# Performance work log

Hardware: AMD Instinct MI355X
Metric: run time of the kernel (lower is better)

The kernel has to match this reference:

```python
import jax, jax.numpy as jnp
import numpy as np
import math

NO, NR, E = 100000, 1000, 1000000
DO, DR, DE, H, OM = 64, 32, 4, 64, 32


def setup_inputs() -> dict:
    key = jax.random.key(0)
    ks = jax.random.split(key, 20)
    s = lambda k, sh: jax.random.normal(k, sh, dtype=jnp.float32) * 0.05
    inp = {
        'x_order': jax.random.normal(ks[0], (NO, DO), dtype=jnp.float32),
        'x_rider': jax.random.normal(ks[1], (NR, DR), dtype=jnp.float32),
        'edge_attr': jax.random.normal(ks[2], (E, DE), dtype=jnp.float32),
        'order_idx': jax.random.randint(ks[3], (E,), 0, NO),
        'rider_idx': jax.random.randint(ks[4], (E,), 0, NR),
        'omega_encoded': jax.random.normal(ks[5], (OM,), dtype=jnp.float32),
        # TransformerConv params (heads=1)
        'Wk': s(ks[6], (DO, H)), 'bk': jnp.zeros((H,), jnp.float32),
        'Wq': s(ks[7], (DR, H)), 'bq': jnp.zeros((H,), jnp.float32),
        'Wv': s(ks[8], (DO, H)), 'bv': jnp.zeros((H,), jnp.float32),
        'We': s(ks[9], (DE, H)),  # lin_edge, bias=False in PyG
        'Wskip': s(ks[10], (DR, H)), 'bskip': jnp.zeros((H,), jnp.float32),
        # order_proj
        'Wp': s(ks[11], (DO, H)), 'bp': jnp.zeros((H,), jnp.float32),
        # residual MLP: Linear(2H+OM,128) -> ReLU -> Linear(128,1)
        'W1': s(ks[12], (2 * H + OM, 128)), 'b1': jnp.zeros((128,), jnp.float32),
        'W2': s(ks[13], (128, 1)), 'b2': jnp.zeros((1,), jnp.float32),
    }
    return inp


def _segment_softmax(alpha, seg, num_segments):
    m = jax.ops.segment_max(alpha, seg, num_segments=num_segments)
    m = jnp.where(jnp.isfinite(m), m, 0.0)
    ex = jnp.exp(alpha - m[seg])
    denom = jax.ops.segment_sum(ex, seg, num_segments=num_segments)
    return ex / (denom[seg] + 1e-16)


def reference(x_order, x_rider, edge_attr, order_idx, rider_idx, omega_encoded,
              Wk, bk, Wq, bq, Wv, bv, We, Wskip, bskip, Wp, bp, W1, b1, W2, b2):
    scale = 1.0 / math.sqrt(H)
    # TransformerConv((order, rider) -> rider), heads=1, edge_dim
    q = x_rider @ Wq + bq            # [NR, H]
    k = x_order @ Wk + bk            # [NO, H]
    v = x_order @ Wv + bv            # [NO, H]
    e = edge_attr @ We               # [E, H]
    k_j = k[order_idx] + e           # [E, H]
    v_j = v[order_idx] + e           # [E, H]
    alpha = jnp.sum(q[rider_idx] * k_j, axis=-1) * scale  # [E]
    alpha = _segment_softmax(alpha, rider_idx, NR)
    agg = jax.ops.segment_sum(alpha[:, None] * v_j, rider_idx, num_segments=NR)  # [NR, H]
    rider_emb = agg + x_rider @ Wskip + bskip  # root/skip connection

    # edge scoring
    order_proj = x_order @ Wp + bp   # [NO, H]
    oe = order_proj[order_idx]       # [E, H]
    re = rider_emb[rider_idx]        # [E, H]
    dot = jnp.sum(oe * re, axis=-1) * scale  # [E]
    omega_expand = jnp.broadcast_to(omega_encoded[None, :], (oe.shape[0], OM))
    resid_in = jnp.concatenate([oe, re, omega_expand], axis=-1)  # [E, 2H+OM]
    hmid = jax.nn.relu(resid_in @ W1 + b1)
    resid = (hmid @ W2 + b2)[:, 0]
    return jnp.clip(dot + resid, -10.0, 10.0)
```

## Files before the change

### kernel.cpp

```cpp
#include <hip/hip_runtime.h>
#include <hip/hip_bf16.h>
#include <math.h>

#define NO_N 100000
#define NR_N 1000
#define E_N  1000000
#define SB     250
#define SCHUNK 4000
#define KVP_TILES 1563

typedef short bf16x8 __attribute__((ext_vector_type(8)));
typedef float floatx4 __attribute__((ext_vector_type(4)));

__device__ __forceinline__ unsigned short bfu(float x) {
    union { __hip_bfloat16 h; unsigned short u; } c;
    c.h = __float2bfloat16(x);
    return c.u;
}
__device__ __forceinline__ float bflo(unsigned int u) {
    return __uint_as_float(u << 16);
}
__device__ __forceinline__ float bfhi(unsigned int u) {
    return __uint_as_float(u & 0xffff0000u);
}

__global__ __launch_bounds__(256) void k_prep_rider(
    const float* __restrict__ xr,
    const float* __restrict__ Wq, const float* __restrict__ bq,
    const float* __restrict__ Wskip, const float* __restrict__ bskip,
    const float* __restrict__ We,
    float* __restrict__ q, float* __restrict__ skip, float* __restrict__ t)
{
    __shared__ float sx[4][32];
    __shared__ float sq[4][64];
    int tid = threadIdx.x;
    int rbase = blockIdx.x * 4;
    if (tid < 128) {
        int rl = tid >> 5, d = tid & 31;
        int r = rbase + rl;
        sx[rl][d] = (r < NR_N) ? xr[r * 32 + d] : 0.f;
    }
    __syncthreads();
    int rl = tid >> 6, h = tid & 63;
    int r = rbase + rl;
    float aq = bq[h], as = bskip[h];
    #pragma unroll 4
    for (int d = 0; d < 32; ++d) {
        float xv = sx[rl][d];
        aq += xv * Wq[d * 64 + h];
        as += xv * Wskip[d * 64 + h];
    }
    sq[rl][h] = aq;
    if (r < NR_N) { q[r * 64 + h] = aq; skip[r * 64 + h] = as; }
    __syncthreads();
    if (tid < 16) {
        int rl2 = tid >> 2, d = tid & 3;
        int r2 = rbase + rl2;
        float acc = 0.f;
        for (int hh = 0; hh < 64; ++hh) acc += We[d * 64 + hh] * sq[rl2][hh];
        if (r2 < NR_N) t[r2 * 4 + d] = acc;
    }
}

__global__ __launch_bounds__(128) void k_prep_b1eff(
    const float* __restrict__ W1, const float* __restrict__ b1,
    const float* __restrict__ omega, float* __restrict__ b1eff)
{
    int c = threadIdx.x;
    float acc = b1[c];
    #pragma unroll 4
    for (int j = 0; j < 32; ++j) acc += omega[j] * W1[(128 + j) * 128 + c];
    b1eff[c] = acc;
}

__global__ __launch_bounds__(256) void k_kvp(
    const float* __restrict__ x,
    const float* __restrict__ Wk, const float* __restrict__ bk,
    const float* __restrict__ Wv, const float* __restrict__ bv,
    const float* __restrict__ Wp, const float* __restrict__ bp,
    unsigned short* __restrict__ kb, unsigned short* __restrict__ vb,
    unsigned short* __restrict__ pb)
{
    __shared__ __align__(16) unsigned short sX[64 * 72];
    const int tid = threadIdx.x;
    const int wave = tid >> 6, lane = tid & 63;
    const int l15 = lane & 15, quad = lane >> 4;

    bf16x8 bfr[3][2];
    float bias[3];
    unsigned short* outT[3];
    int colc[3];
    #pragma unroll
    for (int ct = 0; ct < 3; ++ct) {
        int n = wave * 48 + ct * 16 + l15;
        int table = n >> 6, c = n & 63;
        const float* W  = (table == 0) ? Wk : (table == 1) ? Wv : Wp;
        const float* bb = (table == 0) ? bk : (table == 1) ? bv : bp;
        bias[ct] = bb[c];
        colc[ct] = c;
        outT[ct] = (table == 0) ? kb : (table == 1) ? vb : pb;
        #pragma unroll
        for (int kf = 0; kf < 2; ++kf) {
            bf16x8 f;
            #pragma unroll
            for (int j = 0; j < 8; ++j)
                f[j] = (short)bfu(W[(size_t)(kf * 32 + quad * 8 + j) * 64 + c]);
            bfr[ct][kf] = f;
        }
    }

    const int srl = tid >> 2;
    const int sqt = (tid & 3) * 16;

    for (int tile = blockIdx.x; tile < KVP_TILES; tile += gridDim.x) {
        int rowbase = tile * 64;
        {
            int row = rowbase + srl;
            unsigned short* dst = sX + srl * 72 + sqt;
            if (row < NO_N) {
                const float4* src = (const float4*)(x + (size_t)row * 64 + sqt);
                #pragma unroll
                for (int i = 0; i < 4; ++i) {
                    float4 a = src[i];
                    ushort4 u = { bfu(a.x), bfu(a.y), bfu(a.z), bfu(a.w) };
                    *(ushort4*)(dst + i * 4) = u;
                }
            } else {
                ushort4 z = {0, 0, 0, 0};
                #pragma unroll
                for (int i = 0; i < 4; ++i) *(ushort4*)(dst + i * 4) = z;
            }
        }
        __syncthreads();

        floatx4 acc[4][3];
        #pragma unroll
        for (int rt = 0; rt < 4; ++rt)
            #pragma unroll
            for (int ct = 0; ct < 3; ++ct)
                acc[rt][ct] = (floatx4){bias[ct], bias[ct], bias[ct], bias[ct]};

        #pragma unroll
        for (int rt = 0; rt < 4; ++rt) {
            const unsigned short* ar = sX + (size_t)(rt * 16 + l15) * 72 + quad * 8;
            bf16x8 a0 = *(const bf16x8*)(ar);
            bf16x8 a1 = *(const bf16x8*)(ar + 32);
            #pragma unroll
            for (int ct = 0; ct < 3; ++ct) {
                floatx4 c = acc[rt][ct];
                c = __builtin_amdgcn_mfma_f32_16x16x32_bf16(a0, bfr[ct][0], c, 0, 0, 0);
                c = __builtin_amdgcn_mfma_f32_16x16x32_bf16(a1, bfr[ct][1], c, 0, 0, 0);
                acc[rt][ct] = c;
            }
        }

        #pragma unroll
        for (int rt = 0; rt < 4; ++rt) {
            int rb = rowbase + rt * 16 + quad * 4;
            #pragma unroll
            for (int ct = 0; ct < 3; ++ct) {
                unsigned short* o = outT[ct];
                size_t cbase = colc[ct];
                #pragma unroll
                for (int g = 0; g < 4; ++g) {
                    int row = rb + g;
                    if (row < NO_N)
                        o[(size_t)row * 64 + cbase] = bfu(acc[rt][ct][g]);
                }
            }
        }
        __syncthreads();
    }
}

__global__ __launch_bounds__(256) void k_hist2(const int* __restrict__ ridx,
                                               int* __restrict__ ghist)
{
    __shared__ int hc[NR_N];
    int tid = threadIdx.x, b = blockIdx.x;
    for (int i = tid; i < NR_N; i += 256) hc[i] = 0;
    __syncthreads();
    int s = b * SCHUNK;
    for (int i = s + tid; i < s + SCHUNK; i += 256)
        atomicAdd(&hc[ridx[i]], 1);
    __syncthreads();
    for (int i = tid; i < NR_N; i += 256)
        ghist[i * SB + b] = hc[i];
}

__global__ __launch_bounds__(256) void k_colscan(const int* __restrict__ ghist,
                                                 int* __restrict__ gpre,
                                                 int* __restrict__ counts)
{
    __shared__ int s[256];
    int tid = threadIdx.x, r = blockIdx.x;
    int v = (tid < SB) ? ghist[r * SB + tid] : 0;
    s[tid] = v;
    __syncthreads();
    for (int off = 1; off < 256; off <<= 1) {
        int tv = (tid >= off) ? s[tid - off] : 0;
        __syncthreads();
        s[tid] += tv;
        __syncthreads();
    }
    if (tid < SB) gpre[r * SB + tid] = s[tid] - v;
    if (tid == 255) counts[r] = s[255];
}

__global__ __launch_bounds__(1024) void k_scan(const int* __restrict__ counts,
                                               int* __restrict__ offsets)
{
    __shared__ int s[1024];
    int tid = threadIdx.x;
    int c = (tid < NR_N) ? counts[tid] : 0;
    s[tid] = c;
    __syncthreads();
    for (int off = 1; off < 1024; off <<= 1) {
        int tv = (tid >= off) ? s[tid - off] : 0;
        __syncthreads();
        s[tid] += tv;
        __syncthreads();
    }
    if (tid < NR_N) offsets[tid] = s[tid] - c;
    if (tid == NR_N - 1) offsets[NR_N] = s[tid];
}

__global__ __launch_bounds__(256) void k_scatter2(
    const int* __restrict__ ridx, const int* __restrict__ oidx,
    const float* __restrict__ ea, const float* __restrict__ t,
    const int* __restrict__ offsets, const int* __restrict__ gpre,
    int4* __restrict__ spack)
{
    __shared__ int cur[NR_N];
    int tid = threadIdx.x, b = blockIdx.x;
    for (int i = tid; i < NR_N; i += 256)
        cur[i] = offsets[i] + gpre[i * SB + b];
    __syncthreads();
    int s = b * SCHUNK;
    for (int i = s + tid; i < s + SCHUNK; i += 256) {
        int r = ridx[i];
        float4 e4 = *(const float4*)(ea + (size_t)i * 4);
        float4 t4 = *(const float4*)(t + r * 4);
        float h = e4.x * t4.x + e4.y * t4.y + e4.z * t4.z + e4.w * t4.w;
        int pos = atomicAdd(&cur[r], 1);
        int4 pk;
        pk.x = oidx[i];
        pk.y = __float_as_int(h);
        pk.z = (int)((unsigned)bfu(e4.x) | ((unsigned)bfu(e4.y) << 16));
        pk.w = (int)((unsigned)bfu(e4.z) | ((unsigned)bfu(e4.w) << 16));
        spack[pos] = pk;
    }
}

__global__ __launch_bounds__(1024) void k_rider(
    const int* __restrict__ offsets, const int4* __restrict__ spack,
    const float* __restrict__ q,
    const unsigned short* __restrict__ kb, const unsigned short* __restrict__ vb,
    const float* __restrict__ We, const float* __restrict__ skip,
    float* __restrict__ emb)
{
    __shared__ float sQ[64];
    __shared__ int2 sOX[16][64];
    __shared__ float rv[16][64];
    __shared__ float re4[16][4];
    __shared__ float rd[16];

    int r = blockIdx.x;
    int wave = threadIdx.x >> 6, lane = threadIdx.x & 63;
    if (threadIdx.x < 64) sQ[threadIdx.x] = q[r * 64 + threadIdx.x];
    __syncthreads();

    int beg = offsets[r], end = offsets[r + 1];
    int cnt = end - beg;
    int chunk = (cnt + 15) >> 4;
    int s0 = beg + wave * chunk;
    int s1 = min(s0 + chunk, end);

    float aggv = 0.f, dsum = 0.f;
    float ag0 = 0.f, ag1 = 0.f, ag2 = 0.f, ag3 = 0.f;
    const float2* sQ2 = (const float2*)sQ;

    for (int jb = s0; jb < s1; jb += 64) {
        int j = jb + lane;
        bool valid = (j < s1);
        int4 pk = make_int4(0, 0, 0, 0);
        if (valid) pk = spack[j];
        int oo = pk.x;
        float h = __int_as_float(pk.y);

        const uint4* krow = (const uint4*)(kb + (size_t)oo * 64);
        uint4 K0 = krow[0], K1 = krow[1], K2 = krow[2], K3 = krow[3];
        uint4 K4 = krow[4], K5 = krow[5], K6 = krow[6], K7 = krow[7];
        float acc = h;
        #define DOT8(Kv, base) { \
            float2 qa = sQ2[(base) + 0]; \
            acc = fmaf(bflo(Kv.x), qa.x, acc); acc = fmaf(bfhi(Kv.x), qa.y, acc); \
            float2 qb = sQ2[(base) + 1]; \
            acc = fmaf(bflo(Kv.y), qb.x, acc); acc = fmaf(bfhi(Kv.y), qb.y, acc); \
            float2 qc = sQ2[(base) + 2]; \
            acc = fmaf(bflo(Kv.z), qc.x, acc); acc = fmaf(bfhi(Kv.z), qc.y, acc); \
            float2 qd = sQ2[(base) + 3]; \
            acc = fmaf(bflo(Kv.w), qd.x, acc); acc = fmaf(bfhi(Kv.w), qd.y, acc); }
        DOT8(K0, 0) DOT8(K1, 4) DOT8(K2, 8) DOT8(K3, 12)
        DOT8(K4, 16) DOT8(K5, 20) DOT8(K6, 24) DOT8(K7, 28)
        #undef DOT8

        float exv = valid ? __expf(acc * 0.125f) : 0.f;
        dsum += exv;
        unsigned int ez = (unsigned int)pk.z, ew = (unsigned int)pk.w;
        ag0 = fmaf(exv, bflo(ez), ag0);
        ag1 = fmaf(exv, bfhi(ez), ag1);
        ag2 = fmaf(exv, bflo(ew), ag2);
        ag3 = fmaf(exv, bfhi(ew), ag3);

        sOX[wave][lane] = make_int2(oo, __float_as_int(exv));

        int nn = min(s1 - jb, 64);
        int i = 0;
        for (; i + 8 <= nn; i += 8) {
            int2 x0 = sOX[wave][i + 0], x1 = sOX[wave][i + 1];
            int2 x2 = sOX[wave][i + 2], x3 = sOX[wave][i + 3];
            int2 x4 = sOX[wave][i + 4], x5 = sOX[wave][i + 5];
            int2 x6 = sOX[wave][i + 6], x7 = sOX[wave][i + 7];
            unsigned short u0 = vb[(size_t)x0.x * 64 + lane];
            unsigned short u1 = vb[(size_t)x1.x * 64 + lane];
            unsigned short u2 = vb[(size_t)x2.x * 64 + lane];
            unsigned short u3 = vb[(size_t)x3.x * 64 + lane];
            unsigned short u4 = vb[(size_t)x4.x * 64 + lane];
            unsigned short u5 = vb[(size_t)x5.x * 64 + lane];
            unsigned short u6 = vb[(size_t)x6.x * 64 + lane];
            unsigned short u7 = vb[(size_t)x7.x * 64 + lane];
            aggv = fmaf(__int_as_float(x0.y), __uint_as_float((unsigned int)u0 << 16), aggv);
            aggv = fmaf(__int_as_float(x1.y), __uint_as_float((unsigned int)u1 << 16), aggv);
            aggv = fmaf(__int_as_float(x2.y), __uint_as_float((unsigned int)u2 << 16), aggv);
            aggv = fmaf(__int_as_float(x3.y), __uint_as_float((unsigned int)u3 << 16), aggv);
            aggv = fmaf(__int_as_float(x4.y), __uint_as_float((unsigned int)u4 << 16), aggv);
            aggv = fmaf(__int_as_float(x5.y), __uint_as_float((unsigned int)u5 << 16), aggv);
            aggv = fmaf(__int_as_float(x6.y), __uint_as_float((unsigned int)u6 << 16), aggv);
            aggv = fmaf(__int_as_float(x7.y), __uint_as_float((unsigned int)u7 << 16), aggv);
        }
        for (; i < nn; ++i) {
            int2 xx = sOX[wave][i];
            unsigned short uu = vb[(size_t)xx.x * 64 + lane];
            aggv = fmaf(__int_as_float(xx.y), __uint_as_float((unsigned int)uu << 16), aggv);
        }
    }

    #pragma unroll
    for (int m = 1; m < 64; m <<= 1) {
        dsum += __shfl_xor(dsum, m);
        ag0 += __shfl_xor(ag0, m);
        ag1 += __shfl_xor(ag1, m);
        ag2 += __shfl_xor(ag2, m);
        ag3 += __shfl_xor(ag3, m);
    }

    rv[wave][lane] = aggv;
    if (lane == 0) {
        rd[wave] = dsum;
        re4[wave][0] = ag0; re4[wave][1] = ag1;
        re4[wave][2] = ag2; re4[wave][3] = ag3;
    }
    __syncthreads();
    if (threadIdx.x < 64) {
        int l = threadIdx.x;
        float av = 0.f, ds = 0.f, a0 = 0.f, a1 = 0.f, a2 = 0.f, a3 = 0.f;
        #pragma unroll 4
        for (int w = 0; w < 16; ++w) {
            av += rv[w][l]; ds += rd[w];
            a0 += re4[w][0]; a1 += re4[w][1]; a2 += re4[w][2]; a3 += re4[w][3];
        }
        float corr = a0 * We[0 * 64 + l] + a1 * We[1 * 64 + l]
                   + a2 * We[2 * 64 + l] + a3 * We[3 * 64 + l];
        emb[r * 64 + l] = (av + corr) / (ds + 1e-16f) + skip[r * 64 + l];
    }
}

__global__ __launch_bounds__(256, 4) void k_edge(
    const int* __restrict__ oidx, const int* __restrict__ ridx,
    const unsigned short* __restrict__ pb, const float* __restrict__ emb,
    const float* __restrict__ W1, const float* __restrict__ b1eff,
    const float* __restrict__ W2, const float* __restrict__ b2,
    float* __restrict__ out)
{
    __shared__ __align__(16) unsigned short sA[64 * 136];
    __shared__ float sDot[64];
    __shared__ float sPart[4][64];

    const int tid = threadIdx.x;
    const int wave = tid >> 6;
    const int lane = tid & 63;
    const int l15 = lane & 15;
    const int quad = lane >> 4;

    bf16x8 bfr[2][4];
    float b1v[2], w2v[2];
    #pragma unroll
    for (int ctl = 0; ctl < 2; ++ctl) {
        int n = wave * 32 + ctl * 16 + l15;
        b1v[ctl] = b1eff[n];
        w2v[ctl] = W2[n];
        #pragma unroll
        for (int kc = 0; kc < 4; ++kc) {
            int k0 = kc * 32 + quad * 8;
            bf16x8 f;
            #pragma unroll
            for (int j = 0; j < 8; ++j)
                f[j] = (short)bfu(W1[(size_t)(k0 + j) * 128 + n]);
            bfr[ctl][kc] = f;
        }
    }
    float b2v = b2[0];

    const int el = tid >> 2;
    const int qd = (tid & 3) * 16;

    for (int tile = blockIdx.x; tile < E_N / 64; tile += gridDim.x) {
        int ebase = tile * 64;
        {
            int e = ebase + el;
            int o = oidx[e];
            int r = ridx[e];
            const uint2* po = (const uint2*)(pb + (size_t)o * 64 + qd);
            const float4* pr = (const float4*)(emb + (size_t)r * 64 + qd);
            unsigned short* rowA = sA + el * 136;
            float dotp = 0.f;
            #pragma unroll
            for (int i = 0; i < 4; ++i) {
                uint2 a = po[i];
                float4 b = pr[i];
                dotp += bflo(a.x) * b.x + bfhi(a.x) * b.y
                      + bflo(a.y) * b.z + bfhi(a.y) * b.w;
                *(uint2*)(rowA + qd + i * 4) = a;
                ushort4 ub = { bfu(b.x), bfu(b.y), bfu(b.z), bfu(b.w) };
                *(ushort4*)(rowA + 64 + qd + i * 4) = ub;
            }
            dotp += __shfl_xor(dotp, 1);
            dotp += __shfl_xor(dotp, 2);
            if ((tid & 3) == 0) sDot[el] = dotp;
        }
        __syncthreads();

        floatx4 acc[4][2];
        #pragma unroll
        for (int rt = 0; rt < 4; ++rt)
            #pragma unroll
            for (int ctl = 0; ctl < 2; ++ctl)
                acc[rt][ctl] = (floatx4){0.f, 0.f, 0.f, 0.f};

        #pragma unroll
        for (int rt = 0; rt < 4; ++rt) {
            const unsigned short* ar = sA + (size_t)(rt * 16 + l15) * 136 + quad * 8;
            bf16x8 a0 = *(const bf16x8*)(ar);
            bf16x8 a1 = *(const bf16x8*)(ar + 32);
            bf16x8 a2 = *(const bf16x8*)(ar + 64);
            bf16x8 a3 = *(const bf16x8*)(ar + 96);
            #pragma unroll
            for (int ctl = 0; ctl < 2; ++ctl) {
                floatx4 c = acc[rt][ctl];
                c = __builtin_amdgcn_mfma_f32_16x16x32_bf16(a0, bfr[ctl][0], c, 0, 0, 0);
                c = __builtin_amdgcn_mfma_f32_16x16x32_bf16(a1, bfr[ctl][1], c, 0, 0, 0);
                c = __builtin_amdgcn_mfma_f32_16x16x32_bf16(a2, bfr[ctl][2], c, 0, 0, 0);
                c = __builtin_amdgcn_mfma_f32_16x16x32_bf16(a3, bfr[ctl][3], c, 0, 0, 0);
                acc[rt][ctl] = c;
            }
        }

        #pragma unroll
        for (int rt = 0; rt < 4; ++rt) {
            floatx4 s;
            #pragma unroll
            for (int g = 0; g < 4; ++g)
                s[g] = fmaxf(acc[rt][0][g] + b1v[0], 0.f) * w2v[0]
                     + fmaxf(acc[rt][1][g] + b1v[1], 0.f) * w2v[1];
            #pragma unroll
            for (int m = 1; m < 16; m <<= 1) {
                s[0] += __shfl_xor(s[0], m);
                s[1] += __shfl_xor(s[1], m);
                s[2] += __shfl_xor(s[2], m);
                s[3] += __shfl_xor(s[3], m);
            }
            if (l15 == 0) {
                int rowb = rt * 16 + quad * 4;
                sPart[wave][rowb + 0] = s[0];
                sPart[wave][rowb + 1] = s[1];
                sPart[wave][rowb + 2] = s[2];
                sPart[wave][rowb + 3] = s[3];
            }
        }
        __syncthreads();
        if (tid < 64) {
            float v = sPart[0][tid] + sPart[1][tid] + sPart[2][tid] + sPart[3][tid]
                    + 0.125f * sDot[tid] + b2v;
            out[ebase + tid] = fminf(fmaxf(v, -10.f), 10.f);
        }
        __syncthreads();
    }
}

extern "C" void kernel_launch(void* const* d_in, const int* in_sizes, int n_in,
                              void* d_out, int out_size, void* d_ws, size_t ws_size,
                              hipStream_t stream)
{
    const float* x_order   = (const float*)d_in[0];
    const float* x_rider   = (const float*)d_in[1];
    const float* edge_attr = (const float*)d_in[2];
    const int*   order_idx = (const int*)d_in[3];
    const int*   rider_idx = (const int*)d_in[4];
    const float* omega     = (const float*)d_in[5];
    const float* Wk = (const float*)d_in[6];  const float* bk = (const float*)d_in[7];
    const float* Wq = (const float*)d_in[8];  const float* bq = (const float*)d_in[9];
    const float* Wv = (const float*)d_in[10]; const float* bv = (const float*)d_in[11];
    const float* We = (const float*)d_in[12];
    const float* Wskip = (const float*)d_in[13]; const float* bskip = (const float*)d_in[14];
    const float* Wp = (const float*)d_in[15]; const float* bp = (const float*)d_in[16];
    const float* W1 = (const float*)d_in[17]; const float* b1 = (const float*)d_in[18];
    const float* W2 = (const float*)d_in[19]; const float* b2 = (const float*)d_in[20];
    float* out = (float*)d_out;

    unsigned short* ws_kb = (unsigned short*)d_ws;
    unsigned short* ws_vb = ws_kb + (size_t)NO_N * 64;
    unsigned short* ws_pb = ws_vb + (size_t)NO_N * 64;
    int4* ws_spack = (int4*)(ws_pb + (size_t)NO_N * 64);
    float* wsf     = (float*)(ws_spack + E_N);
    float* ws_q    = wsf;
    float* ws_skip = ws_q + NR_N * 64;
    float* ws_emb  = ws_skip + NR_N * 64;
    float* ws_t    = ws_emb + NR_N * 64;
    float* ws_b1e  = ws_t + NR_N * 4;
    int* ws_counts  = (int*)(ws_b1e + 128);
    int* ws_offsets = ws_counts + NR_N;
    int* ws_ghist   = ws_offsets + NR_N + 8;
    int* ws_gpre    = ws_ghist + NR_N * SB;

    k_prep_rider<<<NR_N / 4, 256, 0, stream>>>(x_rider, Wq, bq, Wskip, bskip, We,
                                               ws_q, ws_skip, ws_t);
    k_prep_b1eff<<<1, 128, 0, stream>>>(W1, b1, omega, ws_b1e);
    k_kvp<<<521, 256, 0, stream>>>(x_order, Wk, bk, Wv, bv, Wp, bp,
                                   ws_kb, ws_vb, ws_pb);
    k_hist2<<<SB, 256, 0, stream>>>(rider_idx, ws_ghist);
    k_colscan<<<NR_N, 256, 0, stream>>>(ws_ghist, ws_gpre, ws_counts);
    k_scan<<<1, 1024, 0, stream>>>(ws_counts, ws_offsets);
    k_scatter2<<<SB, 256, 0, stream>>>(rider_idx, order_idx, edge_attr, ws_t,
                                       ws_offsets, ws_gpre, ws_spack);
    k_rider<<<NR_N, 1024, 0, stream>>>(ws_offsets, ws_spack, ws_q,
                                       ws_kb, ws_vb, We, ws_skip, ws_emb);
    k_edge<<<1024, 256, 0, stream>>>(order_idx, rider_idx, ws_pb, ws_emb,
                                     W1, ws_b1e, W2, b2, out);
}
```

Before: 319.1 us.

## Precompute per-rider MLP contribution and process edges in rider-sorted tiles

Adds a per-rider precompute of emb@W1[64:128]+b1eff (Br), which halves the K dimension of the edge MFMA and removes the rider-embedding half of the staged A tile. The edge kernel now walks rider-grouped tiles built from the existing sort, so each tile shares one rider row and its Br vector. It needs an extra (order, edge) index array written during scatter and a tile-to-rider table built in the scan. The cost is padding tiles per rider, scattered output writes, an extra 8MB write/read, and a serial tile2r fill loop in the single-block scan.

Result: slower. 325.5 us (+2.0%).

```diff
diff --git a/kernel.cpp b/kernel.cpp
--- a/kernel.cpp
+++ b/kernel.cpp
@@ -8,6 +8,7 @@
 #define SB     250
 #define SCHUNK 4000
 #define KVP_TILES 1563
+#define MAXTILES 17008
 
 typedef short bf16x8 __attribute__((ext_vector_type(8)));
 typedef float floatx4 __attribute__((ext_vector_type(4)));
@@ -208,7 +209,9 @@
 }
 
 __global__ __launch_bounds__(1024) void k_scan(const int* __restrict__ counts,
-                                               int* __restrict__ offsets)
+                                               int* __restrict__ offsets,
+                                               int* __restrict__ tilestart,
+                                               int* __restrict__ tile2r)
 {
     __shared__ int s[1024];
     int tid = threadIdx.x;
@@ -223,13 +226,29 @@
     }
     if (tid < NR_N) offsets[tid] = s[tid] - c;
     if (tid == NR_N - 1) offsets[NR_N] = s[tid];
+    __syncthreads();
+    int tc = (tid < NR_N) ? ((c + 63) >> 6) : 0;
+    s[tid] = tc;
+    __syncthreads();
+    for (int off = 1; off < 1024; off <<= 1) {
+        int tv = (tid >= off) ? s[tid - off] : 0;
+        __syncthreads();
+        s[tid] += tv;
+        __syncthreads();
+    }
+    if (tid < NR_N) {
+        int ts = s[tid] - tc;
+        tilestart[tid] = ts;
+        for (int t = 0; t < tc; ++t) tile2r[ts + t] = tid;
+    }
+    if (tid == NR_N - 1) tilestart[NR_N] = s[tid];
 }
 
 __global__ __launch_bounds__(256) void k_scatter2(
     const int* __restrict__ ridx, const int* __restrict__ oidx,
     const float* __restrict__ ea, const float* __restrict__ t,
     const int* __restrict__ offsets, const int* __restrict__ gpre,
-    int4* __restrict__ spack)
+    int4* __restrict__ spack, int2* __restrict__ soe)
 {
     __shared__ int cur[NR_N];
     int tid = threadIdx.x, b = blockIdx.x;
@@ -239,16 +258,18 @@
     int s = b * SCHUNK;
     for (int i = s + tid; i < s + SCHUNK; i += 256) {
         int r = ridx[i];
+        int o = oidx[i];
         float4 e4 = *(const float4*)(ea + (size_t)i * 4);
         float4 t4 = *(const float4*)(t + r * 4);
         float h = e4.x * t4.x + e4.y * t4.y + e4.z * t4.z + e4.w * t4.w;
         int pos = atomicAdd(&cur[r], 1);
         int4 pk;
-        pk.x = oidx[i];
+        pk.x = o;
         pk.y = __float_as_int(h);
         pk.z = (int)((unsigned)bfu(e4.x) | ((unsigned)bfu(e4.y) << 16));
         pk.w = (int)((unsigned)bfu(e4.z) | ((unsigned)bfu(e4.w) << 16));
         spack[pos] = pk;
+        soe[pos] = make_int2(o, i);
     }
 }
 
@@ -376,15 +397,35 @@
     }
 }
 
-__global__ __launch_bounds__(256, 4) void k_edge(
-    const int* __restrict__ oidx, const int* __restrict__ ridx,
+__global__ __launch_bounds__(256) void k_br(
+    const float* __restrict__ emb, const float* __restrict__ W1,
+    const float* __restrict__ b1eff, float* __restrict__ Br)
+{
+    int wave = threadIdx.x >> 6, lane = threadIdx.x & 63;
+    int r = blockIdx.x * 4 + wave;
+    if (r >= NR_N) return;
+    float a0 = b1eff[lane], a1 = b1eff[64 + lane];
+    #pragma unroll 8
+    for (int d = 0; d < 64; ++d) {
+        float ev = emb[r * 64 + d];
+        a0 = fmaf(ev, W1[(size_t)(64 + d) * 128 + lane], a0);
+        a1 = fmaf(ev, W1[(size_t)(64 + d) * 128 + 64 + lane], a1);
+    }
+    Br[r * 128 + lane] = a0;
+    Br[r * 128 + 64 + lane] = a1;
+}
+
+__global__ __launch_bounds__(256) void k_edge2(
+    const int2* __restrict__ soe, const int* __restrict__ offsets,
+    const int* __restrict__ tilestart, const int* __restrict__ tile2r,
     const unsigned short* __restrict__ pb, const float* __restrict__ emb,
-    const float* __restrict__ W1, const float* __restrict__ b1eff,
+    const float* __restrict__ Br, const float* __restrict__ W1,
     const float* __restrict__ W2, const float* __restrict__ b2,
     float* __restrict__ out)
 {
-    __shared__ __align__(16) unsigned short sA[64 * 136];
+    __shared__ __align__(16) unsigned short sA[64 * 72];
     __shared__ float sDot[64];
+    __shared__ int   sE[64];
     __shared__ float sPart[4][64];
 
     const int tid = threadIdx.x;
@@ -393,53 +434,61 @@
     const int l15 = lane & 15;
     const int quad = lane >> 4;
 
-    bf16x8 bfr[2][4];
-    float b1v[2], w2v[2];
+    bf16x8 bfr[2][2];
+    float w2v[2];
     #pragma unroll
     for (int ctl = 0; ctl < 2; ++ctl) {
         int n = wave * 32 + ctl * 16 + l15;
-        b1v[ctl] = b1eff[n];
         w2v[ctl] = W2[n];
         #pragma unroll
-        for (int kc = 0; kc < 4; ++kc) {
-            int k0 = kc * 32 + quad * 8;
+        for (int kc = 0; kc < 2; ++kc) {
             bf16x8 f;
             #pragma unroll
             for (int j = 0; j < 8; ++j)
-                f[j] = (short)bfu(W1[(size_t)(k0 + j) * 128 + n]);
+                f[j] = (short)bfu(W1[(size_t)(kc * 32 + quad * 8 + j) * 128 + n]);
             bfr[ctl][kc] = f;
         }
     }
     float b2v = b2[0];
+    const int ntiles = tilestart[NR_N];
 
     const int el = tid >> 2;
-    const int qd = (tid & 3) * 16;
-
-    for (int tile = blockIdx.x; tile < E_N / 64; tile += gridDim.x) {
-        int ebase = tile * 64;
+    const int q16 = (tid & 3) * 16;
+
+    for (int tile = blockIdx.x; tile < ntiles; tile += gridDim.x) {
+        int r = tile2r[tile];
+        int jb = offsets[r] + ((tile - tilestart[r]) << 6);
+        int jend = offsets[r + 1];
+
         {
-            int e = ebase + el;
-            int o = oidx[e];
-            int r = ridx[e];
-            const uint2* po = (const uint2*)(pb + (size_t)o * 64 + qd);
-            const float4* pr = (const float4*)(emb + (size_t)r * 64 + qd);
-            unsigned short* rowA = sA + el * 136;
-            float dotp = 0.f;
-            #pragma unroll
-            for (int i = 0; i < 4; ++i) {
-                uint2 a = po[i];
-                float4 b = pr[i];
-                dotp += bflo(a.x) * b.x + bfhi(a.x) * b.y
-                      + bflo(a.y) * b.z + bfhi(a.y) * b.w;
-                *(uint2*)(rowA + qd + i * 4) = a;
-                ushort4 ub = { bfu(b.x), bfu(b.y), bfu(b.z), bfu(b.w) };
-                *(ushort4*)(rowA + 64 + qd + i * 4) = ub;
-            }
+            int j = jb + el;
+            int o = 0, e = -1;
+            if (j < jend) { int2 oe = soe[j]; o = oe.x; e = oe.y; }
+            const uint4* po = (const uint4*)(pb + (size_t)o * 64 + q16);
+            uint4 A0 = po[0], A1 = po[1];
+            const float4* pe = (const float4*)(emb + r * 64 + q16);
+            float4 e0 = pe[0], e1 = pe[1], e2 = pe[2], e3 = pe[3];
+            float dotp;
+            dotp  = bflo(A0.x) * e0.x + bfhi(A0.x) * e0.y;
+            dotp += bflo(A0.y) * e0.z + bfhi(A0.y) * e0.w;
+            dotp += bflo(A0.z) * e1.x + bfhi(A0.z) * e1.y;
+            dotp += bflo(A0.w) * e1.z + bfhi(A0.w) * e1.w;
+            dotp += bflo(A1.x) * e2.x + bfhi(A1.x) * e2.y;
+            dotp += bflo(A1.y) * e2.z + bfhi(A1.y) * e2.w;
+            dotp += bflo(A1.z) * e3.x + bfhi(A1.z) * e3.y;
+            dotp += bflo(A1.w) * e3.z + bfhi(A1.w) * e3.w;
+            uint4* sp = (uint4*)(sA + el * 72 + q16);
+            sp[0] = A0; sp[1] = A1;
             dotp += __shfl_xor(dotp, 1);
             dotp += __shfl_xor(dotp, 2);
-            if ((tid & 3) == 0) sDot[el] = dotp;
-        }
-        __syncthreads();
+            if ((tid & 3) == 0) { sDot[el] = dotp; sE[el] = e; }
+        }
+        __syncthreads();
+
+        float brv[2];
+        #pragma unroll
+        for (int ctl = 0; ctl < 2; ++ctl)
+            brv[ctl] = Br[r * 128 + wave * 32 + ctl * 16 + l15];
 
         floatx4 acc[4][2];
         #pragma unroll
@@ -450,18 +499,14 @@
 
         #pragma unroll
         for (int rt = 0; rt < 4; ++rt) {
-            const unsigned short* ar = sA + (size_t)(rt * 16 + l15) * 136 + quad * 8;
+            const unsigned short* ar = sA + (size_t)(rt * 16 + l15) * 72 + quad * 8;
             bf16x8 a0 = *(const bf16x8*)(ar);
             bf16x8 a1 = *(const bf16x8*)(ar + 32);
-            bf16x8 a2 = *(const bf16x8*)(ar + 64);
-            bf16x8 a3 = *(const bf16x8*)(ar + 96);
             #pragma unroll
             for (int ctl = 0; ctl < 2; ++ctl) {
                 floatx4 c = acc[rt][ctl];
                 c = __builtin_amdgcn_mfma_f32_16x16x32_bf16(a0, bfr[ctl][0], c, 0, 0, 0);
                 c = __builtin_amdgcn_mfma_f32_16x16x32_bf16(a1, bfr[ctl][1], c, 0, 0, 0);
-                c = __builtin_amdgcn_mfma_f32_16x16x32_bf16(a2, bfr[ctl][2], c, 0, 0, 0);
-                c = __builtin_amdgcn_mfma_f32_16x16x32_bf16(a3, bfr[ctl][3], c, 0, 0, 0);
                 acc[rt][ctl] = c;
             }
         }
@@ -471,8 +516,8 @@
             floatx4 s;
             #pragma unroll
             for (int g = 0; g < 4; ++g)
-                s[g] = fmaxf(acc[rt][0][g] + b1v[0], 0.f) * w2v[0]
-                     + fmaxf(acc[rt][1][g] + b1v[1], 0.f) * w2v[1];
+                s[g] = fmaxf(acc[rt][0][g] + brv[0], 0.f) * w2v[0]
+                     + fmaxf(acc[rt][1][g] + brv[1], 0.f) * w2v[1];
             #pragma unroll
             for (int m = 1; m < 16; m <<= 1) {
                 s[0] += __shfl_xor(s[0], m);
@@ -490,9 +535,12 @@
         }
         __syncthreads();
         if (tid < 64) {
-            float v = sPart[0][tid] + sPart[1][tid] + sPart[2][tid] + sPart[3][tid]
-                    + 0.125f * sDot[tid] + b2v;
-            out[ebase + tid] = fminf(fmaxf(v, -10.f), 10.f);
+            int e = sE[tid];
+            if (e >= 0) {
+                float v = sPart[0][tid] + sPart[1][tid] + sPart[2][tid] + sPart[3][tid]
+                        + 0.125f * sDot[tid] + b2v;
+                out[e] = fminf(fmaxf(v, -10.f), 10.f);
+            }
         }
         __syncthreads();
     }
@@ -522,15 +570,19 @@
     unsigned short* ws_vb = ws_kb + (size_t)NO_N * 64;
     unsigned short* ws_pb = ws_vb + (size_t)NO_N * 64;
     int4* ws_spack = (int4*)(ws_pb + (size_t)NO_N * 64);
-    float* wsf     = (float*)(ws_spack + E_N);
+    int2* ws_soe   = (int2*)(ws_spack + E_N);
+    float* wsf     = (float*)(ws_soe + E_N);
     float* ws_q    = wsf;
     float* ws_skip = ws_q + NR_N * 64;
     float* ws_emb  = ws_skip + NR_N * 64;
     float* ws_t    = ws_emb + NR_N * 64;
     float* ws_b1e  = ws_t + NR_N * 4;
-    int* ws_counts  = (int*)(ws_b1e + 128);
+    float* ws_Br   = ws_b1e + 128;
+    int* ws_counts  = (int*)(ws_Br + NR_N * 128);
     int* ws_offsets = ws_counts + NR_N;
-    int* ws_ghist   = ws_offsets + NR_N + 8;
+    int* ws_tilest  = ws_offsets + NR_N + 8;
+    int* ws_tile2r  = ws_tilest + NR_N + 8;
+    int* ws_ghist   = ws_tile2r + MAXTILES;
     int* ws_gpre    = ws_ghist + NR_N * SB;
 
     k_prep_rider<<<NR_N / 4, 256, 0, stream>>>(x_rider, Wq, bq, Wskip, bskip, We,
@@ -540,11 +592,12 @@
                                    ws_kb, ws_vb, ws_pb);
     k_hist2<<<SB, 256, 0, stream>>>(rider_idx, ws_ghist);
     k_colscan<<<NR_N, 256, 0, stream>>>(ws_ghist, ws_gpre, ws_counts);
-    k_scan<<<1, 1024, 0, stream>>>(ws_counts, ws_offsets);
+    k_scan<<<1, 1024, 0, stream>>>(ws_counts, ws_offsets, ws_tilest, ws_tile2r);
     k_scatter2<<<SB, 256, 0, stream>>>(rider_idx, order_idx, edge_attr, ws_t,
-                                       ws_offsets, ws_gpre, ws_spack);
+                                       ws_offsets, ws_gpre, ws_spack, ws_soe);
     k_rider<<<NR_N, 1024, 0, stream>>>(ws_offsets, ws_spack, ws_q,
                                        ws_kb, ws_vb, We, ws_skip, ws_emb);
-    k_edge<<<1024, 256, 0, stream>>>(order_idx, rider_idx, ws_pb, ws_emb,
-                                     W1, ws_b1e, W2, b2, out);
-}
+    k_br<<<NR_N / 4, 256, 0, stream>>>(ws_emb, W1, ws_b1e, ws_Br);
+    k_edge2<<<2048, 256, 0, stream>>>(ws_soe, ws_offsets, ws_tilest, ws_tile2r,
+                                      ws_pb, ws_emb, ws_Br, W1, W2, b2, out);
+}
```
